# Optimization experiments

Measured on AMD Instinct MI355X. Metric: run time of the kernel, lower is better.

## Reference

```python
import jax, jax.numpy as jnp
import numpy as np

B, T, C, H = 2, 2048, 1024, 16
D = C // H


def setup_inputs() -> dict:
    key = jax.random.key(0)
    k1, k2, k3 = jax.random.split(key, 3)
    x = jax.random.normal(k1, (B, T, C), dtype=jnp.float32)
    w_attn = jax.random.normal(k2, (3 * C, C), dtype=jnp.float32) * (1.0 / np.sqrt(C))
    w_proj = jax.random.normal(k3, (C, C), dtype=jnp.float32) * (1.0 / np.sqrt(C))
    # causal mask, 1 = keep, 0 = masked (matches att.masked_fill(mask == 0, -inf))
    mask = jnp.tril(jnp.ones((T, T), dtype=jnp.int32))[None, None, :, :]
    return {"x": x, "w_attn": w_attn, "w_proj": w_proj, "mask": mask}


def reference(x, w_attn, w_proj, mask):
    Bq, Tq, Cq = x.shape
    qkv = x @ w_attn.T                      # [B,T,3C] (torch Linear: x @ W^T)
    q, k, v = jnp.split(qkv, 3, axis=2)
    # [B,T,C] -> [B,H,T,D]
    q = q.reshape(Bq, Tq, H, D).transpose(0, 2, 1, 3)
    k = k.reshape(Bq, Tq, H, D).transpose(0, 2, 1, 3)
    v = v.reshape(Bq, Tq, H, D).transpose(0, 2, 1, 3)
    att = jnp.einsum("bhqd,bhkd->bhqk", q, k) * (1.0 / np.sqrt(D))
    att = jnp.where(mask == 0, -jnp.inf, att)
    att = jax.nn.softmax(att, axis=-1)      # dropout p=0.0 -> identity
    y = jnp.einsum("bhqk,bhkd->bhqd", att, v)
    y = y.transpose(0, 2, 1, 3).reshape(Bq, Tq, Cq)
    return y @ w_proj.T
```

## Files before the change

### kernel.cpp

```cpp
#include <hip/hip_runtime.h>
#include <hip/hip_bf16.h>
#include <math.h>


typedef __attribute__((ext_vector_type(4))) float floatx4;
typedef __attribute__((ext_vector_type(8))) __bf16 bf16x8;

#define MFMA_BF16(a, b, c) __builtin_amdgcn_mfma_f32_16x16x32_bf16((a), (b), (c), 0, 0, 0)

typedef __attribute__((address_space(1))) const uint32_t* gas_t;
typedef __attribute__((address_space(3))) uint32_t* las_t;
__device__ inline void gl2lds16(const void* g, void* l) {
    __builtin_amdgcn_global_load_lds((gas_t)g, (las_t)l, 16, 0, 0);
}

__device__ inline uint4 cvt8_f32_bf16(const float4 a, const float4 b) {
    union { __hip_bfloat16 h[8]; uint4 u; } c;
    c.h[0] = __float2bfloat16(a.x); c.h[1] = __float2bfloat16(a.y);
    c.h[2] = __float2bfloat16(a.z); c.h[3] = __float2bfloat16(a.w);
    c.h[4] = __float2bfloat16(b.x); c.h[5] = __float2bfloat16(b.y);
    c.h[6] = __float2bfloat16(b.z); c.h[7] = __float2bfloat16(b.w);
    return c.u;
}

__global__ __launch_bounds__(256) void cvt_f32_bf16_k(
    const float* __restrict__ in, __hip_bfloat16* __restrict__ out, int n)
{
    const int i = (blockIdx.x * 256 + threadIdx.x) * 8;
    if (i < n) {
        const float4 a = *(const float4*)&in[i];
        const float4 b = *(const float4*)&in[i + 4];
        *(uint4*)&out[i] = cvt8_f32_bf16(a, b);
    }
}

template<bool C_F32>
__global__ __launch_bounds__(256) void gemm_bt_mfma(
    const __hip_bfloat16* __restrict__ A,
    const __hip_bfloat16* __restrict__ Bt,
    void* __restrict__ Cv, int M, int N, int K)
{
    __shared__ __hip_bfloat16 As[128][32];
    __shared__ __hip_bfloat16 Bs[128][32];

    const int tid  = threadIdx.x;
    const int wave = tid >> 6;
    const int lane = tid & 63;
    const int quad = lane >> 4;
    const int l15  = lane & 15;
    const int wrow = wave >> 1;
    const int wcol = wave & 1;
    const int bm = blockIdx.y * 128;
    const int bn = blockIdx.x * 128;

    floatx4 acc[4][4];
#pragma unroll
    for (int i = 0; i < 4; ++i)
#pragma unroll
        for (int j = 0; j < 4; ++j)
            acc[i][j] = (floatx4){0.f, 0.f, 0.f, 0.f};

    const int srow = lane >> 2;
    const int scol = (lane & 3) * 8;

    const __hip_bfloat16* Abase = A  + (size_t)bm * K;
    const __hip_bfloat16* Bbase = Bt + (size_t)bn * K;

    for (int k0 = 0; k0 < K; k0 += 32) {
#pragma unroll
        for (int c = 0; c < 2; ++c) {
            const int rbase = wave * 32 + c * 16;
            gl2lds16(&Abase[(size_t)(rbase + srow) * K + k0 + scol], &As[rbase][0]);
            gl2lds16(&Bbase[(size_t)(rbase + srow) * K + k0 + scol], &Bs[rbase][0]);
        }
        __syncthreads();

        bf16x8 af[4], bfv[4];
#pragma unroll
        for (int i = 0; i < 4; ++i)
            af[i] = *(const bf16x8*)&As[wrow * 64 + i * 16 + l15][quad * 8];
#pragma unroll
        for (int j = 0; j < 4; ++j)
            bfv[j] = *(const bf16x8*)&Bs[wcol * 64 + j * 16 + l15][quad * 8];

#pragma unroll
        for (int i = 0; i < 4; ++i)
#pragma unroll
            for (int j = 0; j < 4; ++j)
                acc[i][j] = MFMA_BF16(af[i], bfv[j], acc[i][j]);
        __syncthreads();
    }

#pragma unroll
    for (int i = 0; i < 4; ++i)
#pragma unroll
        for (int j = 0; j < 4; ++j)
#pragma unroll
            for (int r = 0; r < 4; ++r) {
                const int row = bm + wrow * 64 + i * 16 + quad * 4 + r;
                const int col = bn + wcol * 64 + j * 16 + l15;
                if (C_F32)
                    ((float*)Cv)[(size_t)row * N + col] = acc[i][j][r];
                else
                    ((__hip_bfloat16*)Cv)[(size_t)row * N + col] = __float2bfloat16(acc[i][j][r]);
            }
}

__global__ __launch_bounds__(256) void transpose_v(
    const __hip_bfloat16* __restrict__ qkv, __hip_bfloat16* __restrict__ VtT)
{
    __shared__ __hip_bfloat16 Ls[64][72];
    const int b = blockIdx.z, h = blockIdx.y, t0 = blockIdx.x * 64;
    const int tid = threadIdx.x;
    {
        const int r = tid >> 2, c = (tid & 3) * 16;
        const size_t g = ((size_t)(b * 2048 + t0 + r)) * 3072 + 2048 + h * 64 + c;
        *(uint4*)&Ls[r][c]     = *(const uint4*)&qkv[g];
        *(uint4*)&Ls[r][c + 8] = *(const uint4*)&qkv[g + 8];
    }
    __syncthreads();
    {
        const int d = tid >> 2, k0 = (tid & 3) * 16;
        __hip_bfloat16 tmp[16];
#pragma unroll
        for (int j = 0; j < 16; ++j) tmp[j] = Ls[k0 + j][d];
        const size_t g = ((size_t)((b * 16 + h) * 64 + d)) * 2048 + t0 + k0;
        *(uint4*)&VtT[g]     = *(uint4*)&tmp[0];
        *(uint4*)&VtT[g + 8] = *(uint4*)&tmp[8];
    }
}

struct QState {
    bf16x8  aq[2];
    float   m[4], l[4];
    floatx4 acc[4];
};

__device__ inline void attn_softmax_tile(
    QState& st, bool diag,
    const __hip_bfloat16 (*Ks)[72], __hip_bfloat16 (*Ps)[72],
    int wave, int quad, int l15)
{
    floatx4 s[4];
#pragma unroll
    for (int jt = 0; jt < 4; ++jt) s[jt] = (floatx4){0.f, 0.f, 0.f, 0.f};
#pragma unroll
    for (int jt = 0; jt < 4; ++jt)
#pragma unroll
        for (int kd = 0; kd < 2; ++kd) {
            bf16x8 bk = *(const bf16x8*)&Ks[jt * 16 + l15][kd * 32 + quad * 8];
            s[jt] = MFMA_BF16(st.aq[kd], bk, s[jt]);
        }

    float mx[4];
#pragma unroll
    for (int r = 0; r < 4; ++r) mx[r] = -INFINITY;
#pragma unroll
    for (int jt = 0; jt < 4; ++jt)
#pragma unroll
        for (int r = 0; r < 4; ++r) {
            float v = s[jt][r] * 0.125f;
            if (diag && (jt * 16 + l15) > (wave * 16 + quad * 4 + r)) v = -INFINITY;
            s[jt][r] = v;
            mx[r] = fmaxf(mx[r], v);
        }
#pragma unroll
    for (int o = 8; o >= 1; o >>= 1)
#pragma unroll
        for (int r = 0; r < 4; ++r) mx[r] = fmaxf(mx[r], __shfl_xor(mx[r], o));

    float alpha[4], rs[4];
#pragma unroll
    for (int r = 0; r < 4; ++r) {
        const float mn = fmaxf(st.m[r], mx[r]);
        alpha[r] = __expf(st.m[r] - mn);
        st.m[r] = mn;
        rs[r] = 0.f;
    }
#pragma unroll
    for (int jt = 0; jt < 4; ++jt)
#pragma unroll
        for (int r = 0; r < 4; ++r) {
            const float p = __expf(s[jt][r] - st.m[r]);
            s[jt][r] = p;
            rs[r] += p;
        }
#pragma unroll
    for (int o = 8; o >= 1; o >>= 1)
#pragma unroll
        for (int r = 0; r < 4; ++r) rs[r] += __shfl_xor(rs[r], o);
#pragma unroll
    for (int r = 0; r < 4; ++r) st.l[r] = st.l[r] * alpha[r] + rs[r];

#pragma unroll
    for (int jt = 0; jt < 4; ++jt)
#pragma unroll
        for (int r = 0; r < 4; ++r)
            Ps[wave * 16 + quad * 4 + r][jt * 16 + l15] = __float2bfloat16(s[jt][r]);

#pragma unroll
    for (int jd = 0; jd < 4; ++jd)
#pragma unroll
        for (int r = 0; r < 4; ++r) st.acc[jd][r] *= alpha[r];
}

__device__ inline void attn_pv_tile(
    QState& st, const __hip_bfloat16 (*Ps)[72], const __hip_bfloat16 (*Vt)[72],
    int wave, int quad, int l15)
{
#pragma unroll
    for (int kk = 0; kk < 2; ++kk) {
        bf16x8 ap = *(const bf16x8*)&Ps[wave * 16 + l15][kk * 32 + quad * 8];
#pragma unroll
        for (int jd = 0; jd < 4; ++jd) {
            bf16x8 bv = *(const bf16x8*)&Vt[jd * 16 + l15][kk * 32 + quad * 8];
            st.acc[jd] = MFMA_BF16(ap, bv, st.acc[jd]);
        }
    }
}

__global__ __launch_bounds__(256) void attn_kernel(
    const __hip_bfloat16* __restrict__ qkv,
    const __hip_bfloat16* __restrict__ VtT,
    __hip_bfloat16* __restrict__ y)
{
    constexpr int T = 2048;
    __shared__ __hip_bfloat16 Ks[64][72];
    __shared__ __hip_bfloat16 Vt[64][72];
    __shared__ __hip_bfloat16 PsA[64][72];
    __shared__ __hip_bfloat16 PsB[64][72];

    const int b = blockIdx.z, h = blockIdx.y, p = blockIdx.x;
    const int q0A = p * 64;
    const int q0B = (31 - p) * 64;

    const int tid  = threadIdx.x;
    const int wave = tid >> 6;
    const int lane = tid & 63;
    const int quad = lane >> 4;
    const int l15  = lane & 15;

    const __hip_bfloat16* base  = qkv + (size_t)b * T * 3072;
    const __hip_bfloat16* vbase = VtT + (size_t)((b * 16 + h) * 64) * 2048;

    QState A, Bq;
#pragma unroll
    for (int kd = 0; kd < 2; ++kd) {
        A.aq[kd]  = *(const bf16x8*)&base[(size_t)(q0A + wave * 16 + l15) * 3072 + h * 64 + kd * 32 + quad * 8];
        Bq.aq[kd] = *(const bf16x8*)&base[(size_t)(q0B + wave * 16 + l15) * 3072 + h * 64 + kd * 32 + quad * 8];
    }
#pragma unroll
    for (int r = 0; r < 4; ++r) {
        A.m[r] = -INFINITY; A.l[r] = 0.f;
        Bq.m[r] = -INFINITY; Bq.l[r] = 0.f;
        A.acc[r] = (floatx4){0.f, 0.f, 0.f, 0.f};
        Bq.acc[r] = (floatx4){0.f, 0.f, 0.f, 0.f};
    }

    for (int j0 = 0; j0 <= q0B; j0 += 64) {
        const bool actA = (j0 <= q0A);
        {
            const int r = tid >> 2, cg = (tid & 3) * 16;
            const size_t kg = (size_t)(j0 + r) * 3072 + 1024 + h * 64 + cg;
            *(uint4*)&Ks[r][cg]     = *(const uint4*)&base[kg];
            *(uint4*)&Ks[r][cg + 8] = *(const uint4*)&base[kg + 8];
            const size_t vg = (size_t)r * 2048 + j0 + cg;
            *(uint4*)&Vt[r][cg]     = *(const uint4*)&vbase[vg];
            *(uint4*)&Vt[r][cg + 8] = *(const uint4*)&vbase[vg + 8];
        }
        __syncthreads();

        attn_softmax_tile(Bq, j0 == q0B, Ks, PsB, wave, quad, l15);
        if (actA) attn_softmax_tile(A, j0 == q0A, Ks, PsA, wave, quad, l15);
        __syncthreads();

        attn_pv_tile(Bq, PsB, Vt, wave, quad, l15);
        if (actA) attn_pv_tile(A, PsA, Vt, wave, quad, l15);
        __syncthreads();
    }

#pragma unroll
    for (int jd = 0; jd < 4; ++jd)
#pragma unroll
        for (int r = 0; r < 4; ++r) {
            const int col = h * 64 + jd * 16 + l15;
            const int rowA = q0A + wave * 16 + quad * 4 + r;
            y[((size_t)b * T + rowA) * 1024 + col] = __float2bfloat16(A.acc[jd][r] / A.l[r]);
            const int rowB = q0B + wave * 16 + quad * 4 + r;
            y[((size_t)b * T + rowB) * 1024 + col] = __float2bfloat16(Bq.acc[jd][r] / Bq.l[r]);
        }
}

extern "C" void kernel_launch(void* const* d_in, const int* in_sizes, int n_in,
                              void* d_out, int out_size, void* d_ws, size_t ws_size,
                              hipStream_t stream)
{
    const float* x      = (const float*)d_in[0];
    const float* w_attn = (const float*)d_in[1];
    const float* w_proj = (const float*)d_in[2];

    float* out = (float*)d_out;
    __hip_bfloat16* xb  = (__hip_bfloat16*)d_ws;
    __hip_bfloat16* wab = xb  + (size_t)4096 * 1024;
    __hip_bfloat16* wpb = wab + (size_t)3072 * 1024;
    __hip_bfloat16* qkv = wpb + (size_t)1024 * 1024;
    __hip_bfloat16* y   = qkv + (size_t)4096 * 3072;
    __hip_bfloat16* vt  = y   + (size_t)4096 * 1024;

    cvt_f32_bf16_k<<<2048, 256, 0, stream>>>(x,      xb,  4096 * 1024);
    cvt_f32_bf16_k<<<1536, 256, 0, stream>>>(w_attn, wab, 3072 * 1024);
    cvt_f32_bf16_k<<<512,  256, 0, stream>>>(w_proj, wpb, 1024 * 1024);

    gemm_bt_mfma<false><<<dim3(24, 32), 256, 0, stream>>>(xb, wab, qkv, 4096, 3072, 1024);

    transpose_v<<<dim3(32, 16, 2), 256, 0, stream>>>(qkv, vt);
    attn_kernel<<<dim3(16, 16, 2), 256, 0, stream>>>(qkv, vt, y);

    gemm_bt_mfma<true><<<dim3(8, 32), 256, 0, stream>>>(y, wpb, out, 4096, 1024, 1024);
}
```

Measured before the change: 237.2 us.

## Double-buffer K/V in attention, interleave paired query tiles, add narrower output-projection GEMM

The attention kernel now double-buffers the K and V^T tiles in shared memory. The next tile is prefetched into registers while the current one is computed, which removes one barrier per iteration. The two paired query tiles share each K/V fragment load, and their MFMAs are interleaved. Grid order is changed so batch and head vary fastest. The output projection switches to a new 128x64-tile GEMM, doubling block count for better CU occupancy at the cost of less reuse per block.

```diff
diff --git a/kernel.cpp b/kernel.cpp
--- a/kernel.cpp
+++ b/kernel.cpp
@@ -106,6 +106,75 @@
             }
 }
 
+__global__ __launch_bounds__(256) void gemm_bt_mfma_n64(
+    const __hip_bfloat16* __restrict__ A,
+    const __hip_bfloat16* __restrict__ Bt,
+    float* __restrict__ C, int M, int N, int K)
+{
+    __shared__ __hip_bfloat16 As[128][32];
+    __shared__ __hip_bfloat16 Bs[64][32];
+
+    const int tid  = threadIdx.x;
+    const int wave = tid >> 6;
+    const int lane = tid & 63;
+    const int quad = lane >> 4;
+    const int l15  = lane & 15;
+    const int wrow = wave >> 1;
+    const int wcol = wave & 1;
+    const int bm = blockIdx.y * 128;
+    const int bn = blockIdx.x * 64;
+
+    floatx4 acc[4][2];
+#pragma unroll
+    for (int i = 0; i < 4; ++i)
+#pragma unroll
+        for (int j = 0; j < 2; ++j)
+            acc[i][j] = (floatx4){0.f, 0.f, 0.f, 0.f};
+
+    const int srow = lane >> 2;
+    const int scol = (lane & 3) * 8;
+
+    const __hip_bfloat16* Abase = A  + (size_t)bm * K;
+    const __hip_bfloat16* Bbase = Bt + (size_t)bn * K;
+
+    for (int k0 = 0; k0 < K; k0 += 32) {
+        {
+            const int ra0 = wave * 32;
+            gl2lds16(&Abase[(size_t)(ra0 + srow) * K + k0 + scol], &As[ra0][0]);
+            gl2lds16(&Abase[(size_t)(ra0 + 16 + srow) * K + k0 + scol], &As[ra0 + 16][0]);
+            const int rb0 = wave * 16;
+            gl2lds16(&Bbase[(size_t)(rb0 + srow) * K + k0 + scol], &Bs[rb0][0]);
+        }
+        __syncthreads();
+
+        bf16x8 af[4], bfv[2];
+#pragma unroll
+        for (int i = 0; i < 4; ++i)
+            af[i] = *(const bf16x8*)&As[wrow * 64 + i * 16 + l15][quad * 8];
+#pragma unroll
+        for (int j = 0; j < 2; ++j)
+            bfv[j] = *(const bf16x8*)&Bs[wcol * 32 + j * 16 + l15][quad * 8];
+
+#pragma unroll
+        for (int i = 0; i < 4; ++i)
+#pragma unroll
+            for (int j = 0; j < 2; ++j)
+                acc[i][j] = MFMA_BF16(af[i], bfv[j], acc[i][j]);
+        __syncthreads();
+    }
+
+#pragma unroll
+    for (int i = 0; i < 4; ++i)
+#pragma unroll
+        for (int j = 0; j < 2; ++j)
+#pragma unroll
+            for (int r = 0; r < 4; ++r) {
+                const int row = bm + wrow * 64 + i * 16 + quad * 4 + r;
+                const int col = bn + wcol * 32 + j * 16 + l15;
+                C[(size_t)row * N + col] = acc[i][j][r];
+            }
+}
+
 __global__ __launch_bounds__(256) void transpose_v(
     const __hip_bfloat16* __restrict__ qkv, __hip_bfloat16* __restrict__ VtT)
 {
@@ -130,107 +199,19 @@
     }
 }
 
-struct QState {
-    bf16x8  aq[2];
-    float   m[4], l[4];
-    floatx4 acc[4];
-};
-
-__device__ inline void attn_softmax_tile(
-    QState& st, bool diag,
-    const __hip_bfloat16 (*Ks)[72], __hip_bfloat16 (*Ps)[72],
-    int wave, int quad, int l15)
-{
-    floatx4 s[4];
-#pragma unroll
-    for (int jt = 0; jt < 4; ++jt) s[jt] = (floatx4){0.f, 0.f, 0.f, 0.f};
-#pragma unroll
-    for (int jt = 0; jt < 4; ++jt)
-#pragma unroll
-        for (int kd = 0; kd < 2; ++kd) {
-            bf16x8 bk = *(const bf16x8*)&Ks[jt * 16 + l15][kd * 32 + quad * 8];
-            s[jt] = MFMA_BF16(st.aq[kd], bk, s[jt]);
-        }
-
-    float mx[4];
-#pragma unroll
-    for (int r = 0; r < 4; ++r) mx[r] = -INFINITY;
-#pragma unroll
-    for (int jt = 0; jt < 4; ++jt)
-#pragma unroll
-        for (int r = 0; r < 4; ++r) {
-            float v = s[jt][r] * 0.125f;
-            if (diag && (jt * 16 + l15) > (wave * 16 + quad * 4 + r)) v = -INFINITY;
-            s[jt][r] = v;
-            mx[r] = fmaxf(mx[r], v);
-        }
-#pragma unroll
-    for (int o = 8; o >= 1; o >>= 1)
-#pragma unroll
-        for (int r = 0; r < 4; ++r) mx[r] = fmaxf(mx[r], __shfl_xor(mx[r], o));
-
-    float alpha[4], rs[4];
-#pragma unroll
-    for (int r = 0; r < 4; ++r) {
-        const float mn = fmaxf(st.m[r], mx[r]);
-        alpha[r] = __expf(st.m[r] - mn);
-        st.m[r] = mn;
-        rs[r] = 0.f;
-    }
-#pragma unroll
-    for (int jt = 0; jt < 4; ++jt)
-#pragma unroll
-        for (int r = 0; r < 4; ++r) {
-            const float p = __expf(s[jt][r] - st.m[r]);
-            s[jt][r] = p;
-            rs[r] += p;
-        }
-#pragma unroll
-    for (int o = 8; o >= 1; o >>= 1)
-#pragma unroll
-        for (int r = 0; r < 4; ++r) rs[r] += __shfl_xor(rs[r], o);
-#pragma unroll
-    for (int r = 0; r < 4; ++r) st.l[r] = st.l[r] * alpha[r] + rs[r];
-
-#pragma unroll
-    for (int jt = 0; jt < 4; ++jt)
-#pragma unroll
-        for (int r = 0; r < 4; ++r)
-            Ps[wave * 16 + quad * 4 + r][jt * 16 + l15] = __float2bfloat16(s[jt][r]);
-
-#pragma unroll
-    for (int jd = 0; jd < 4; ++jd)
-#pragma unroll
-        for (int r = 0; r < 4; ++r) st.acc[jd][r] *= alpha[r];
-}
-
-__device__ inline void attn_pv_tile(
-    QState& st, const __hip_bfloat16 (*Ps)[72], const __hip_bfloat16 (*Vt)[72],
-    int wave, int quad, int l15)
-{
-#pragma unroll
-    for (int kk = 0; kk < 2; ++kk) {
-        bf16x8 ap = *(const bf16x8*)&Ps[wave * 16 + l15][kk * 32 + quad * 8];
-#pragma unroll
-        for (int jd = 0; jd < 4; ++jd) {
-            bf16x8 bv = *(const bf16x8*)&Vt[jd * 16 + l15][kk * 32 + quad * 8];
-            st.acc[jd] = MFMA_BF16(ap, bv, st.acc[jd]);
-        }
-    }
-}
-
 __global__ __launch_bounds__(256) void attn_kernel(
     const __hip_bfloat16* __restrict__ qkv,
     const __hip_bfloat16* __restrict__ VtT,
     __hip_bfloat16* __restrict__ y)
 {
     constexpr int T = 2048;
-    __shared__ __hip_bfloat16 Ks[64][72];
-    __shared__ __hip_bfloat16 Vt[64][72];
-    __shared__ __hip_bfloat16 PsA[64][72];
-    __shared__ __hip_bfloat16 PsB[64][72];
-
-    const int b = blockIdx.z, h = blockIdx.y, p = blockIdx.x;
+    __shared__ __hip_bfloat16 Ks[2][64][72];
+    __shared__ __hip_bfloat16 Vt[2][64][72];
+    __shared__ __hip_bfloat16 Ps[2][64][72];
+
+    const int bh = blockIdx.x;
+    const int b = bh >> 4, h = bh & 15;
+    const int p = blockIdx.y;
     const int q0A = p * 64;
     const int q0B = (31 - p) * 64;
 
@@ -243,40 +224,185 @@
     const __hip_bfloat16* base  = qkv + (size_t)b * T * 3072;
     const __hip_bfloat16* vbase = VtT + (size_t)((b * 16 + h) * 64) * 2048;
 
-    QState A, Bq;
+    bf16x8 aqA[2], aqB[2];
 #pragma unroll
     for (int kd = 0; kd < 2; ++kd) {
-        A.aq[kd]  = *(const bf16x8*)&base[(size_t)(q0A + wave * 16 + l15) * 3072 + h * 64 + kd * 32 + quad * 8];
-        Bq.aq[kd] = *(const bf16x8*)&base[(size_t)(q0B + wave * 16 + l15) * 3072 + h * 64 + kd * 32 + quad * 8];
-    }
+        aqA[kd] = *(const bf16x8*)&base[(size_t)(q0A + wave * 16 + l15) * 3072 + h * 64 + kd * 32 + quad * 8];
+        aqB[kd] = *(const bf16x8*)&base[(size_t)(q0B + wave * 16 + l15) * 3072 + h * 64 + kd * 32 + quad * 8];
+    }
+
+    float mA[4], lA[4], mB[4], lB[4];
+    floatx4 accA[4], accB[4];
 #pragma unroll
     for (int r = 0; r < 4; ++r) {
-        A.m[r] = -INFINITY; A.l[r] = 0.f;
-        Bq.m[r] = -INFINITY; Bq.l[r] = 0.f;
-        A.acc[r] = (floatx4){0.f, 0.f, 0.f, 0.f};
-        Bq.acc[r] = (floatx4){0.f, 0.f, 0.f, 0.f};
-    }
-
+        mA[r] = -INFINITY; lA[r] = 0.f; mB[r] = -INFINITY; lB[r] = 0.f;
+        accA[r] = (floatx4){0.f, 0.f, 0.f, 0.f};
+        accB[r] = (floatx4){0.f, 0.f, 0.f, 0.f};
+    }
+
+    const int sr = tid >> 2;
+    const int sc = (tid & 3) * 16;
+
+    {
+        const size_t kg = (size_t)sr * 3072 + 1024 + h * 64 + sc;
+        const size_t vg = (size_t)sr * 2048 + 0 + sc;
+        *(uint4*)&Ks[0][sr][sc]     = *(const uint4*)&base[kg];
+        *(uint4*)&Ks[0][sr][sc + 8] = *(const uint4*)&base[kg + 8];
+        *(uint4*)&Vt[0][sr][sc]     = *(const uint4*)&vbase[vg];
+        *(uint4*)&Vt[0][sr][sc + 8] = *(const uint4*)&vbase[vg + 8];
+    }
+    __syncthreads();
+
+    int cur = 0;
     for (int j0 = 0; j0 <= q0B; j0 += 64) {
-        const bool actA = (j0 <= q0A);
+        const bool actA  = (j0 <= q0A);
+        const bool dgA   = (j0 == q0A);
+        const bool dgB   = (j0 == q0B);
+        const bool hnext = (j0 + 64 <= q0B);
+
+        uint4 pk0, pk1, pv0, pv1;
+        if (hnext) {
+            const size_t kg = (size_t)(j0 + 64 + sr) * 3072 + 1024 + h * 64 + sc;
+            const size_t vg = (size_t)sr * 2048 + (j0 + 64) + sc;
+            pk0 = *(const uint4*)&base[kg];
+            pk1 = *(const uint4*)&base[kg + 8];
+            pv0 = *(const uint4*)&vbase[vg];
+            pv1 = *(const uint4*)&vbase[vg + 8];
+        }
+
+        floatx4 sA[4], sB[4];
+#pragma unroll
+        for (int jt = 0; jt < 4; ++jt) {
+            sA[jt] = (floatx4){0.f, 0.f, 0.f, 0.f};
+            sB[jt] = (floatx4){0.f, 0.f, 0.f, 0.f};
+        }
+#pragma unroll
+        for (int jt = 0; jt < 4; ++jt)
+#pragma unroll
+            for (int kd = 0; kd < 2; ++kd) {
+                bf16x8 bk = *(const bf16x8*)&Ks[cur][jt * 16 + l15][kd * 32 + quad * 8];
+                sB[jt] = MFMA_BF16(aqB[kd], bk, sB[jt]);
+                if (actA) sA[jt] = MFMA_BF16(aqA[kd], bk, sA[jt]);
+            }
+
         {
-            const int r = tid >> 2, cg = (tid & 3) * 16;
-            const size_t kg = (size_t)(j0 + r) * 3072 + 1024 + h * 64 + cg;
-            *(uint4*)&Ks[r][cg]     = *(const uint4*)&base[kg];
-            *(uint4*)&Ks[r][cg + 8] = *(const uint4*)&base[kg + 8];
-            const size_t vg = (size_t)r * 2048 + j0 + cg;
-            *(uint4*)&Vt[r][cg]     = *(const uint4*)&vbase[vg];
-            *(uint4*)&Vt[r][cg + 8] = *(const uint4*)&vbase[vg + 8];
-        }
-        __syncthreads();
-
-        attn_softmax_tile(Bq, j0 == q0B, Ks, PsB, wave, quad, l15);
-        if (actA) attn_softmax_tile(A, j0 == q0A, Ks, PsA, wave, quad, l15);
-        __syncthreads();
-
-        attn_pv_tile(Bq, PsB, Vt, wave, quad, l15);
-        if (actA) attn_pv_tile(A, PsA, Vt, wave, quad, l15);
-        __syncthreads();
+            float mx[4];
+#pragma unroll
+            for (int r = 0; r < 4; ++r) mx[r] = -INFINITY;
+#pragma unroll
+            for (int jt = 0; jt < 4; ++jt)
+#pragma unroll
+                for (int r = 0; r < 4; ++r) {
+                    float v = sB[jt][r] * 0.125f;
+                    if (dgB && (jt * 16 + l15) > (wave * 16 + quad * 4 + r)) v = -INFINITY;
+                    sB[jt][r] = v;
+                    mx[r] = fmaxf(mx[r], v);
+                }
+#pragma unroll
+            for (int o = 8; o >= 1; o >>= 1)
+#pragma unroll
+                for (int r = 0; r < 4; ++r) mx[r] = fmaxf(mx[r], __shfl_xor(mx[r], o));
+            float alpha[4], rs[4];
+#pragma unroll
+            for (int r = 0; r < 4; ++r) {
+                const float mn = fmaxf(mB[r], mx[r]);
+                alpha[r] = __expf(mB[r] - mn);
+                mB[r] = mn; rs[r] = 0.f;
+            }
+#pragma unroll
+            for (int jt = 0; jt < 4; ++jt)
+#pragma unroll
+                for (int r = 0; r < 4; ++r) {
+                    const float pp = __expf(sB[jt][r] - mB[r]);
+                    sB[jt][r] = pp; rs[r] += pp;
+                }
+#pragma unroll
+            for (int o = 8; o >= 1; o >>= 1)
+#pragma unroll
+                for (int r = 0; r < 4; ++r) rs[r] += __shfl_xor(rs[r], o);
+#pragma unroll
+            for (int r = 0; r < 4; ++r) lB[r] = lB[r] * alpha[r] + rs[r];
+#pragma unroll
+            for (int jt = 0; jt < 4; ++jt)
+#pragma unroll
+                for (int r = 0; r < 4; ++r)
+                    Ps[1][wave * 16 + quad * 4 + r][jt * 16 + l15] = __float2bfloat16(sB[jt][r]);
+#pragma unroll
+            for (int jd = 0; jd < 4; ++jd)
+#pragma unroll
+                for (int r = 0; r < 4; ++r) accB[jd][r] *= alpha[r];
+        }
+        if (actA) {
+            float mx[4];
+#pragma unroll
+            for (int r = 0; r < 4; ++r) mx[r] = -INFINITY;
+#pragma unroll
+            for (int jt = 0; jt < 4; ++jt)
+#pragma unroll
+                for (int r = 0; r < 4; ++r) {
+                    float v = sA[jt][r] * 0.125f;
+                    if (dgA && (jt * 16 + l15) > (wave * 16 + quad * 4 + r)) v = -INFINITY;
+                    sA[jt][r] = v;
+                    mx[r] = fmaxf(mx[r], v);
+                }
+#pragma unroll
+            for (int o = 8; o >= 1; o >>= 1)
+#pragma unroll
+                for (int r = 0; r < 4; ++r) mx[r] = fmaxf(mx[r], __shfl_xor(mx[r], o));
+            float alpha[4], rs[4];
+#pragma unroll
+            for (int r = 0; r < 4; ++r) {
+                const float mn = fmaxf(mA[r], mx[r]);
+                alpha[r] = __expf(mA[r] - mn);
+                mA[r] = mn; rs[r] = 0.f;
+            }
+#pragma unroll
+            for (int jt = 0; jt < 4; ++jt)
+#pragma unroll
+                for (int r = 0; r < 4; ++r) {
+                    const float pp = __expf(sA[jt][r] - mA[r]);
+                    sA[jt][r] = pp; rs[r] += pp;
+                }
+#pragma unroll
+            for (int o = 8; o >= 1; o >>= 1)
+#pragma unroll
+                for (int r = 0; r < 4; ++r) rs[r] += __shfl_xor(rs[r], o);
+#pragma unroll
+            for (int r = 0; r < 4; ++r) lA[r] = lA[r] * alpha[r] + rs[r];
+#pragma unroll
+            for (int jt = 0; jt < 4; ++jt)
+#pragma unroll
+                for (int r = 0; r < 4; ++r)
+                    Ps[0][wave * 16 + quad * 4 + r][jt * 16 + l15] = __float2bfloat16(sA[jt][r]);
+#pragma unroll
+            for (int jd = 0; jd < 4; ++jd)
+#pragma unroll
+                for (int r = 0; r < 4; ++r) accA[jd][r] *= alpha[r];
+        }
+
+        if (hnext) {
+            const int nxt = cur ^ 1;
+            *(uint4*)&Ks[nxt][sr][sc]     = pk0;
+            *(uint4*)&Ks[nxt][sr][sc + 8] = pk1;
+            *(uint4*)&Vt[nxt][sr][sc]     = pv0;
+            *(uint4*)&Vt[nxt][sr][sc + 8] = pv1;
+        }
+        __syncthreads();
+
+#pragma unroll
+        for (int kk = 0; kk < 2; ++kk) {
+            bf16x8 apB = *(const bf16x8*)&Ps[1][wave * 16 + l15][kk * 32 + quad * 8];
+            bf16x8 apA;
+            if (actA) apA = *(const bf16x8*)&Ps[0][wave * 16 + l15][kk * 32 + quad * 8];
+#pragma unroll
+            for (int jd = 0; jd < 4; ++jd) {
+                bf16x8 bv = *(const bf16x8*)&Vt[cur][jd * 16 + l15][kk * 32 + quad * 8];
+                accB[jd] = MFMA_BF16(apB, bv, accB[jd]);
+                if (actA) accA[jd] = MFMA_BF16(apA, bv, accA[jd]);
+            }
+        }
+        __syncthreads();
+        cur ^= 1;
     }
 
 #pragma unroll
@@ -285,9 +411,9 @@
         for (int r = 0; r < 4; ++r) {
             const int col = h * 64 + jd * 16 + l15;
             const int rowA = q0A + wave * 16 + quad * 4 + r;
-            y[((size_t)b * T + rowA) * 1024 + col] = __float2bfloat16(A.acc[jd][r] / A.l[r]);
+            y[((size_t)b * T + rowA) * 1024 + col] = __float2bfloat16(accA[jd][r] / lA[r]);
             const int rowB = q0B + wave * 16 + quad * 4 + r;
-            y[((size_t)b * T + rowB) * 1024 + col] = __float2bfloat16(Bq.acc[jd][r] / Bq.l[r]);
+            y[((size_t)b * T + rowB) * 1024 + col] = __float2bfloat16(accB[jd][r] / lB[r]);
         }
 }
 
@@ -314,7 +440,7 @@
     gemm_bt_mfma<false><<<dim3(24, 32), 256, 0, stream>>>(xb, wab, qkv, 4096, 3072, 1024);
 
     transpose_v<<<dim3(32, 16, 2), 256, 0, stream>>>(qkv, vt);
-    attn_kernel<<<dim3(16, 16, 2), 256, 0, stream>>>(qkv, vt, y);
-
-    gemm_bt_mfma<true><<<dim3(8, 32), 256, 0, stream>>>(y, wpb, out, 4096, 1024, 1024);
-}
+    attn_kernel<<<dim3(32, 16), 256, 0, stream>>>(qkv, vt, y);
+
+    gemm_bt_mfma_n64<<<dim3(16, 32), 256, 0, stream>>>(y, wpb, out, 4096, 1024, 1024);
+}
```

New measurement: 238.2 us. About the same (+0.4%).
